# Performance work log

Hardware: AMD Instinct MI355X
Metric: run time of the kernel (lower is better)

Reference implementation:

```python
import jax, jax.numpy as jnp
import numpy as np
from jax import lax

CAM_EDGE = 4096


def setup_inputs() -> dict:
    key = jax.random.key(0)
    x1 = jax.random.normal(key, (CAM_EDGE, CAM_EDGE), dtype=jnp.float32)
    return {"x1": x1}


def _label_components(mask):
    """4-connected component labeling via iterative min-label propagation.

    mask: [E, E] bool. Returns int32 [E, E] labels: each masked cell gets the
    minimum linear index of its connected component; unmasked cells get the
    sentinel N = E*E.
    """
    E = mask.shape[0]
    N = E * E
    sent = jnp.int32(N)
    init = jnp.where(mask, jnp.arange(N, dtype=jnp.int32).reshape(E, E), sent)
    sent_row = jnp.full((1, E), sent, dtype=jnp.int32)
    sent_col = jnp.full((E, 1), sent, dtype=jnp.int32)

    def propagate(lab):
        dn = jnp.concatenate([sent_row, lab[:-1]], axis=0)   # neighbor from above
        up = jnp.concatenate([lab[1:], sent_row], axis=0)    # neighbor from below
        lf = jnp.concatenate([sent_col, lab[:, :-1]], axis=1)
        rt = jnp.concatenate([lab[:, 1:], sent_col], axis=1)
        m = jnp.minimum(jnp.minimum(lab, up), jnp.minimum(dn, jnp.minimum(lf, rt)))
        return jnp.where(mask, m, sent)

    def cond(carry):
        _, changed = carry
        return changed

    def body(carry):
        lab, _ = carry
        new = propagate(lab)
        return new, jnp.any(new != lab)

    labels, _ = lax.while_loop(cond, body, (init, jnp.array(True)))
    return labels


def reference(x1):
    E = x1.shape[0]
    N = E * E
    v = jnp.tanh(x1)
    mask = v > 0
    labels = _label_components(mask)          # [E, E] int32, sentinel N for masked-out
    flat_lab = labels.reshape(-1)
    vflat = jnp.where(mask, v, 0.0).reshape(-1)
    ones = mask.reshape(-1).astype(v.dtype)
    # bucket N+1 collects the sentinel (non-positive cells); drop it
    sums = jax.ops.segment_sum(vflat, flat_lab, num_segments=N + 1)[:N]
    counts = jax.ops.segment_sum(ones, flat_lab, num_segments=N + 1)[:N]
    has = counts > 0                          # one True per connected component (its root index)
    per_comp = jnp.where(has, sums / (N + 1 - counts), 0.0)
    n_comp = jnp.sum(has.astype(v.dtype))
    total = jnp.sum(per_comp)
    return jnp.where(n_comp > 0, total / n_comp, 0.0)
```

## Files before the change

kernel.cpp:

```cpp
#include <hip/hip_runtime.h>

#define EDGE 4096
#define NPIX (EDGE * EDGE)
#define NTILES 4096
#define SLOTS 2048
#define PREP_BLOCKS 2048

typedef unsigned long long u64;

static __device__ __forceinline__ int g_load(int* L, int i) {
    return __hip_atomic_load(&L[i], __ATOMIC_RELAXED, __HIP_MEMORY_SCOPE_AGENT);
}
static __device__ __forceinline__ void g_store(int* L, int i, int v) {
    __hip_atomic_store(&L[i], v, __ATOMIC_RELAXED, __HIP_MEMORY_SCOPE_AGENT);
}
static __device__ int g_find(int* L, int i) {
    while (true) {
        const int p = g_load(L, i);
        if (p == i) return i;
        const int gp = g_load(L, p);
        if (gp == p) return p;
        g_store(L, i, gp);
        i = gp;
    }
}
static __device__ int g_unite(int* L, int a, int b) {
    while (true) {
        a = g_find(L, a); b = g_find(L, b);
        if (a == b) return 0;
        const int lo = a < b ? a : b;
        const int hi = a ^ b ^ lo;
        const int old = atomicMin(&L[hi], lo);
        if (old == hi) return 1;
        a = lo; b = old;
    }
}

static __device__ __forceinline__ int l_load(int* L, int i) {
    return __hip_atomic_load(&L[i], __ATOMIC_RELAXED, __HIP_MEMORY_SCOPE_WORKGROUP);
}
static __device__ __forceinline__ void l_store(int* L, int i, int v) {
    __hip_atomic_store(&L[i], v, __ATOMIC_RELAXED, __HIP_MEMORY_SCOPE_WORKGROUP);
}
static __device__ int l_find(int* L, int i) {
    while (true) {
        const int p = l_load(L, i);
        if (p == i) return i;
        const int gp = l_load(L, p);
        if (gp == p) return p;
        l_store(L, i, gp);
        i = gp;
    }
}
static __device__ void l_unite(int* L, int a, int b) {
    while (true) {
        a = l_find(L, a); b = l_find(L, b);
        if (a == b) return;
        const int lo = a < b ? a : b;
        const int hi = a ^ b ^ lo;
        const int old = atomicMin(&L[hi], lo);
        if (old == hi) return;
        a = lo; b = old;
    }
}

__global__ __launch_bounds__(256) void k_prep(const float* __restrict__ x,
                                              unsigned char* __restrict__ maskb,
                                              double* __restrict__ partials) {
    __shared__ float wsumf[4];
    float sf = 0.0f;
    const int stride = gridDim.x * blockDim.x;
    for (int p = blockIdx.x * blockDim.x + threadIdx.x; p < NPIX / 8; p += stride) {
        const float4 a0 = reinterpret_cast<const float4*>(x)[p * 2];
        const float4 a1 = reinterpret_cast<const float4*>(x)[p * 2 + 1];
        const float v[8] = {a0.x, a0.y, a0.z, a0.w, a1.x, a1.y, a1.z, a1.w};
        unsigned int m = 0;
        #pragma unroll
        for (int j = 0; j < 8; ++j) {
            const float vj = v[j];
            if (vj > 0.0f) {
                m |= 1u << j;
                const float e = __expf(2.0f * vj);
                sf += 1.0f - 2.0f * __builtin_amdgcn_rcpf(e + 1.0f);
            }
        }
        maskb[p] = (unsigned char)m;
    }
    for (int off = 32; off > 0; off >>= 1) sf += __shfl_down(sf, off, 64);
    if ((threadIdx.x & 63) == 0) wsumf[threadIdx.x >> 6] = sf;
    __syncthreads();
    if (threadIdx.x == 0)
        partials[blockIdx.x] =
            (double)wsumf[0] + (double)wsumf[1] + (double)wsumf[2] + (double)wsumf[3];
}

__global__ __launch_bounds__(256) void k_ccl(const u64* __restrict__ M,
                                             int* __restrict__ G,
                                             int* __restrict__ topM, int* __restrict__ botM,
                                             int* __restrict__ leftM, int* __restrict__ rightM,
                                             int* __restrict__ rootsArr) {
    __shared__ u64 mrow[64];
    __shared__ u64 rstart[64];
    __shared__ int rowbase[64];
    __shared__ int P[SLOTS];
    __shared__ int wtot[4];
    __shared__ int Rtot;
    const int t = threadIdx.x;
    const int tile = blockIdx.x;
    const int tr = tile >> 6, tc = tile & 63;

    if (t < 64) {
        const u64 m = M[(((tr << 6) | t) << 6) | tc];
        mrow[t] = m;
        const u64 rs = m & ~(m << 1);
        rstart[t] = rs;
        int inc = __popcll(rs);
        const int nr = inc;
        #pragma unroll
        for (int off = 1; off < 64; off <<= 1) {
            const int v = __shfl_up(inc, off, 64);
            if (t >= off) inc += v;
        }
        rowbase[t] = inc - nr;
        if (t == 63) Rtot = inc;
    }
    #pragma unroll
    for (int i = t; i < SLOTS; i += 256) P[i] = i;
    __syncthreads();

    {
        const int rr = t >> 2;
        if (rr >= 1) {
            const u64 vm = mrow[rr] & mrow[rr - 1];
            u64 st = vm & ~(vm << 1);
            const int cb = (t & 3) * 16;
            st = (st >> cb) & 0xFFFFull;
            if (st) {
                const u64 rs  = rstart[rr];
                const u64 rsu = rstart[rr - 1];
                const int rb  = rowbase[rr];
                const int rbu = rowbase[rr - 1];
                do {
                    const int j = __builtin_ctzll(st) + cb;
                    const u64 thru = ~0ull >> (63 - j);
                    const int na = rb  + __popcll(rs  & thru) - 1;
                    const int nb = rbu + __popcll(rsu & thru) - 1;
                    const int old = atomicMin(&P[na], nb);
                    if (old != na && old != nb) l_unite(P, nb, old);
                    st &= st - 1;
                } while (st);
            }
        }
    }
    __syncthreads();

    const int R = Rtot;
    int broot = -1;
    {
        int rr, j;
        if (t < 64)       { rr = 0;       j = t; }
        else if (t < 128) { rr = 63;      j = t - 64; }
        else if (t < 192) { rr = t - 128; j = 0; }
        else              { rr = t - 192; j = 63; }
        if ((mrow[rr] >> j) & 1ull) {
            const int idx = __popcll(rstart[rr] & (~0ull >> (63 - j))) - 1;
            broot = l_find(P, rowbase[rr] + idx);
        }
    }
    int c = 0;
    for (int i = t; i < R; i += 256) c += (P[i] == i);
    int inc2 = c;
    #pragma unroll
    for (int off = 1; off < 64; off <<= 1) {
        const int v = __shfl_up(inc2, off, 64);
        if ((t & 63) >= off) inc2 += v;
    }
    if ((t & 63) == 63) wtot[t >> 6] = inc2;
    __syncthreads();

    const int w = t >> 6;
    int wbase = 0;
    if (w > 0) wbase += wtot[0];
    if (w > 1) wbase += wtot[1];
    if (w > 2) wbase += wtot[2];
    const int my_base = wbase + inc2 - c;
    const int nroots = wtot[0] + wtot[1] + wtot[2] + wtot[3];
    const int tileBase = tile * SLOTS;
    {
        int k = my_base;
        for (int i = t; i < R; i += 256) if (P[i] == i) P[i] = k++;
    }
    for (int i = t; i < nroots; i += 256) G[tileBase + i] = tileBase + i;
    __syncthreads();

    {
        const int node = (broot >= 0) ? (tileBase + P[broot]) : -1;
        const int bi = (tile << 6) | (t & 63);
        if (t < 64)       topM[bi]   = node;
        else if (t < 128) botM[bi]   = node;
        else if (t < 192) leftM[bi]  = node;
        else              rightM[bi] = node;
    }
    if (t == 0) rootsArr[tile] = nroots;
}

__global__ __launch_bounds__(128) void k_xmerge(const int* __restrict__ topM,
                                                const int* __restrict__ botM,
                                                const int* __restrict__ leftM,
                                                const int* __restrict__ rightM,
                                                int* G, int* __restrict__ linksArr) {
    __shared__ int lsum[2];
    const int t = threadIdx.x, tile = blockIdx.x;
    const int tr = tile >> 6, tc = tile & 63;
    int links = 0;
    if (t < 64) {
        if (tr > 0) {
            const int a = topM[(tile << 6) | t];
            const int b = botM[((tile - 64) << 6) | t];
            const int ap = __shfl_up(a, 1, 64);
            const int bp = __shfl_up(b, 1, 64);
            if ((a | b) >= 0) {
                const bool redund = (t > 0) && ((ap | bp) >= 0);
                if (!redund) links = g_unite(G, a, b);
            }
        }
    } else {
        const int rr = t - 64;
        if (tc > 0) {
            const int a = leftM[(tile << 6) | rr];
            const int b = rightM[((tile - 1) << 6) | rr];
            const int ap = __shfl_up(a, 1, 64);
            const int bp = __shfl_up(b, 1, 64);
            if ((a | b) >= 0) {
                const bool redund = (rr > 0) && ((ap | bp) >= 0);
                if (!redund) links = g_unite(G, a, b);
            }
        }
    }
    for (int off = 32; off > 0; off >>= 1) links += __shfl_down(links, off, 64);
    if ((t & 63) == 0) lsum[t >> 6] = links;
    __syncthreads();
    if (t == 0) linksArr[tile] = lsum[0] + lsum[1];
}

__global__ __launch_bounds__(256) void k_final(const double* __restrict__ partials,
                                               const int* __restrict__ rootsArr,
                                               const int* __restrict__ linksArr,
                                               float* __restrict__ out) {
    __shared__ double sd[256];
    __shared__ int si[256];
    const int t = threadIdx.x;
    double s = 0.0; int n = 0;
    for (int i = t; i < PREP_BLOCKS; i += 256) s += partials[i];
    for (int i = t; i < NTILES; i += 256) n += rootsArr[i] - linksArr[i];
    sd[t] = s; si[t] = n; __syncthreads();
    for (int off = 128; off > 0; off >>= 1) {
        if (t < off) { sd[t] += sd[t + off]; si[t] += si[t + off]; }
        __syncthreads();
    }
    if (t == 0) {
        const int nn = si[0];
        out[0] = (nn > 0) ? (float)(sd[0] / (double)(NPIX + 1) / (double)nn) : 0.0f;
    }
}

extern "C" void kernel_launch(void* const* d_in, const int* in_sizes, int n_in,
                              void* d_out, int out_size, void* d_ws, size_t ws_size,
                              hipStream_t stream) {
    const float* x = (const float*)d_in[0];
    float* out = (float*)d_out;

    char* ws = (char*)d_ws;
    int* G = (int*)ws;
    int* topM   = (int*)(ws + (32u << 20));
    int* botM   = topM  + NTILES * 64;
    int* leftM  = botM  + NTILES * 64;
    int* rightM = leftM + NTILES * 64;
    unsigned char* maskb = (unsigned char*)(ws + (36u << 20));
    double* partials = (double*)(ws + (38u << 20));
    int* rootsArr = (int*)(ws + (38u << 20) + (64u << 10));
    int* linksArr = (int*)(ws + (38u << 20) + (80u << 10));

    k_prep  <<<PREP_BLOCKS, 256, 0, stream>>>(x, maskb, partials);
    k_ccl   <<<NTILES, 256, 0, stream>>>((const u64*)maskb, G,
                                         topM, botM, leftM, rightM, rootsArr);
    k_xmerge<<<NTILES, 128, 0, stream>>>(topM, botM, leftM, rightM, G, linksArr);
    k_final <<<1, 256, 0, stream>>>(partials, rootsArr, linksArr, out);
}
```

Baseline: 59.51 us.

## Process one tile per wavefront in CCL and merge, with tile-major mask layout

The prep kernel now writes the bit mask in a tile-major layout, so each tile's 64 row words sit next to each other and load in one coalesced read. The local labeling kernel now gives each 64x64 tile to a single wavefront, four tiles per block. Row data moves between lanes by shuffle instead of shared memory, and wave barriers replace block-wide __syncthreads. The cross-tile merge kernel also handles one tile per wave, with each lane doing both the vertical and horizontal edges. This removes block synchronisation and raises work per block, but each wave now serialises the row-union loop that four threads per row used to share, and it uses 32KB of LDS per block.

```diff
diff --git a/kernel.cpp b/kernel.cpp
--- a/kernel.cpp
+++ b/kernel.cpp
@@ -84,7 +84,9 @@
                 sf += 1.0f - 2.0f * __builtin_amdgcn_rcpf(e + 1.0f);
             }
         }
-        maskb[p] = (unsigned char)m;
+        const int row = p >> 9, cp = p & 511;
+        const int tile = ((row >> 6) << 6) | (cp >> 3);
+        maskb[((size_t)tile << 9) | ((row & 63) << 3) | (cp & 7)] = (unsigned char)m;
     }
     for (int off = 32; off > 0; off >>= 1) sf += __shfl_down(sf, off, 64);
     if ((threadIdx.x & 63) == 0) wsumf[threadIdx.x >> 6] = sf;
@@ -99,148 +101,111 @@
                                              int* __restrict__ topM, int* __restrict__ botM,
                                              int* __restrict__ leftM, int* __restrict__ rightM,
                                              int* __restrict__ rootsArr) {
-    __shared__ u64 mrow[64];
-    __shared__ u64 rstart[64];
-    __shared__ int rowbase[64];
-    __shared__ int P[SLOTS];
-    __shared__ int wtot[4];
-    __shared__ int Rtot;
-    const int t = threadIdx.x;
-    const int tile = blockIdx.x;
-    const int tr = tile >> 6, tc = tile & 63;
-
-    if (t < 64) {
-        const u64 m = M[(((tr << 6) | t) << 6) | tc];
-        mrow[t] = m;
-        const u64 rs = m & ~(m << 1);
-        rstart[t] = rs;
-        int inc = __popcll(rs);
-        const int nr = inc;
-        #pragma unroll
-        for (int off = 1; off < 64; off <<= 1) {
-            const int v = __shfl_up(inc, off, 64);
-            if (t >= off) inc += v;
-        }
-        rowbase[t] = inc - nr;
-        if (t == 63) Rtot = inc;
-    }
+    __shared__ int Pall[4][SLOTS];
+    const int lane = threadIdx.x & 63;
+    const int w = threadIdx.x >> 6;
+    const int tile = (blockIdx.x << 2) | w;
+    int* P = Pall[w];
+
+    const u64 m = M[(tile << 6) | lane];
+    const u64 rs = m & ~(m << 1);
+    const int nr = __popcll(rs);
+    int inc = nr;
     #pragma unroll
-    for (int i = t; i < SLOTS; i += 256) P[i] = i;
-    __syncthreads();
-
-    {
-        const int rr = t >> 2;
-        if (rr >= 1) {
-            const u64 vm = mrow[rr] & mrow[rr - 1];
-            u64 st = vm & ~(vm << 1);
-            const int cb = (t & 3) * 16;
-            st = (st >> cb) & 0xFFFFull;
-            if (st) {
-                const u64 rs  = rstart[rr];
-                const u64 rsu = rstart[rr - 1];
-                const int rb  = rowbase[rr];
-                const int rbu = rowbase[rr - 1];
-                do {
-                    const int j = __builtin_ctzll(st) + cb;
-                    const u64 thru = ~0ull >> (63 - j);
-                    const int na = rb  + __popcll(rs  & thru) - 1;
-                    const int nb = rbu + __popcll(rsu & thru) - 1;
-                    const int old = atomicMin(&P[na], nb);
-                    if (old != na && old != nb) l_unite(P, nb, old);
-                    st &= st - 1;
-                } while (st);
-            }
-        }
-    }
-    __syncthreads();
-
-    const int R = Rtot;
-    int broot = -1;
-    {
-        int rr, j;
-        if (t < 64)       { rr = 0;       j = t; }
-        else if (t < 128) { rr = 63;      j = t - 64; }
-        else if (t < 192) { rr = t - 128; j = 0; }
-        else              { rr = t - 192; j = 63; }
-        if ((mrow[rr] >> j) & 1ull) {
-            const int idx = __popcll(rstart[rr] & (~0ull >> (63 - j))) - 1;
-            broot = l_find(P, rowbase[rr] + idx);
-        }
-    }
+    for (int off = 1; off < 64; off <<= 1) {
+        const int v = __shfl_up(inc, off, 64);
+        if (lane >= off) inc += v;
+    }
+    const int rowbase = inc - nr;
+    const int R = __shfl(inc, 63, 64);
+
+    #pragma unroll
+    for (int q = 0; q < SLOTS / 64; ++q) P[(q << 6) | lane] = (q << 6) | lane;
+    __builtin_amdgcn_wave_barrier();
+
+    const u64 mu  = __shfl_up(m, 1, 64);
+    const u64 rsu = __shfl_up(rs, 1, 64);
+    const int rbu = __shfl_up(rowbase, 1, 64);
+    if (lane >= 1) {
+        const u64 vm = m & mu;
+        u64 st = vm & ~(vm << 1);
+        while (st) {
+            const int j = __builtin_ctzll(st);
+            const u64 thru = ~0ull >> (63 - j);
+            const int na = rowbase + __popcll(rs  & thru) - 1;
+            const int nb = rbu     + __popcll(rsu & thru) - 1;
+            const int old = atomicMin(&P[na], nb);
+            if (old != na && old != nb) l_unite(P, nb, old);
+            st &= st - 1;
+        }
+    }
+    __builtin_amdgcn_wave_barrier();
+
+    const u64 m0  = __shfl((long long)m, 0, 64),  rs0  = __shfl((long long)rs, 0, 64);
+    const u64 m63 = __shfl((long long)m, 63, 64), rs63 = __shfl((long long)rs, 63, 64);
+    const int rb63 = __shfl(rowbase, 63, 64);
+    const u64 thruL = ~0ull >> (63 - lane);
+    int bt = -1, bb = -1, bl = -1, br = -1;
+    if ((m0 >> lane) & 1ull)  bt = l_find(P, __popcll(rs0 & thruL) - 1);
+    if ((m63 >> lane) & 1ull) bb = l_find(P, rb63 + __popcll(rs63 & thruL) - 1);
+    if (m & 1ull)             bl = l_find(P, rowbase);
+    if ((m >> 63) & 1ull)     br = l_find(P, rowbase + nr - 1);
+    __builtin_amdgcn_wave_barrier();
+
     int c = 0;
-    for (int i = t; i < R; i += 256) c += (P[i] == i);
+    for (int i = lane; i < R; i += 64) c += (P[i] == i);
     int inc2 = c;
     #pragma unroll
     for (int off = 1; off < 64; off <<= 1) {
         const int v = __shfl_up(inc2, off, 64);
-        if ((t & 63) >= off) inc2 += v;
-    }
-    if ((t & 63) == 63) wtot[t >> 6] = inc2;
-    __syncthreads();
-
-    const int w = t >> 6;
-    int wbase = 0;
-    if (w > 0) wbase += wtot[0];
-    if (w > 1) wbase += wtot[1];
-    if (w > 2) wbase += wtot[2];
-    const int my_base = wbase + inc2 - c;
-    const int nroots = wtot[0] + wtot[1] + wtot[2] + wtot[3];
+        if (lane >= off) inc2 += v;
+    }
+    const int nroots = __shfl(inc2, 63, 64);
+    int k = inc2 - c;
+    for (int i = lane; i < R; i += 64) if (P[i] == i) P[i] = k++;
+    __builtin_amdgcn_wave_barrier();
+
     const int tileBase = tile * SLOTS;
-    {
-        int k = my_base;
-        for (int i = t; i < R; i += 256) if (P[i] == i) P[i] = k++;
-    }
-    for (int i = t; i < nroots; i += 256) G[tileBase + i] = tileBase + i;
-    __syncthreads();
-
-    {
-        const int node = (broot >= 0) ? (tileBase + P[broot]) : -1;
-        const int bi = (tile << 6) | (t & 63);
-        if (t < 64)       topM[bi]   = node;
-        else if (t < 128) botM[bi]   = node;
-        else if (t < 192) leftM[bi]  = node;
-        else              rightM[bi] = node;
-    }
-    if (t == 0) rootsArr[tile] = nroots;
-}
-
-__global__ __launch_bounds__(128) void k_xmerge(const int* __restrict__ topM,
+    for (int i = lane; i < nroots; i += 64) G[tileBase + i] = tileBase + i;
+
+    const int bi = (tile << 6) | lane;
+    topM[bi]   = (bt >= 0) ? (tileBase + P[bt]) : -1;
+    botM[bi]   = (bb >= 0) ? (tileBase + P[bb]) : -1;
+    leftM[bi]  = (bl >= 0) ? (tileBase + P[bl]) : -1;
+    rightM[bi] = (br >= 0) ? (tileBase + P[br]) : -1;
+    if (lane == 0) rootsArr[tile] = nroots;
+}
+
+__global__ __launch_bounds__(256) void k_xmerge(const int* __restrict__ topM,
                                                 const int* __restrict__ botM,
                                                 const int* __restrict__ leftM,
                                                 const int* __restrict__ rightM,
                                                 int* G, int* __restrict__ linksArr) {
-    __shared__ int lsum[2];
-    const int t = threadIdx.x, tile = blockIdx.x;
+    const int lane = threadIdx.x & 63;
+    const int w = threadIdx.x >> 6;
+    const int tile = (blockIdx.x << 2) | w;
     const int tr = tile >> 6, tc = tile & 63;
     int links = 0;
-    if (t < 64) {
-        if (tr > 0) {
-            const int a = topM[(tile << 6) | t];
-            const int b = botM[((tile - 64) << 6) | t];
-            const int ap = __shfl_up(a, 1, 64);
-            const int bp = __shfl_up(b, 1, 64);
-            if ((a | b) >= 0) {
-                const bool redund = (t > 0) && ((ap | bp) >= 0);
-                if (!redund) links = g_unite(G, a, b);
-            }
-        }
-    } else {
-        const int rr = t - 64;
-        if (tc > 0) {
-            const int a = leftM[(tile << 6) | rr];
-            const int b = rightM[((tile - 1) << 6) | rr];
-            const int ap = __shfl_up(a, 1, 64);
-            const int bp = __shfl_up(b, 1, 64);
-            if ((a | b) >= 0) {
-                const bool redund = (rr > 0) && ((ap | bp) >= 0);
-                if (!redund) links = g_unite(G, a, b);
-            }
+    {
+        int a = -1, b = -1;
+        if (tr > 0) { a = topM[(tile << 6) | lane]; b = botM[((tile - 64) << 6) | lane]; }
+        const int ap = __shfl_up(a, 1, 64), bp = __shfl_up(b, 1, 64);
+        if (tr > 0 && (a | b) >= 0) {
+            const bool red = (lane > 0) && ((ap | bp) >= 0);
+            if (!red) links += g_unite(G, a, b);
+        }
+    }
+    {
+        int a = -1, b = -1;
+        if (tc > 0) { a = leftM[(tile << 6) | lane]; b = rightM[((tile - 1) << 6) | lane]; }
+        const int ap = __shfl_up(a, 1, 64), bp = __shfl_up(b, 1, 64);
+        if (tc > 0 && (a | b) >= 0) {
+            const bool red = (lane > 0) && ((ap | bp) >= 0);
+            if (!red) links += g_unite(G, a, b);
         }
     }
     for (int off = 32; off > 0; off >>= 1) links += __shfl_down(links, off, 64);
-    if ((t & 63) == 0) lsum[t >> 6] = links;
-    __syncthreads();
-    if (t == 0) linksArr[tile] = lsum[0] + lsum[1];
+    if (lane == 0) linksArr[tile] = links;
 }
 
 __global__ __launch_bounds__(256) void k_final(const double* __restrict__ partials,
@@ -282,8 +247,8 @@
     int* linksArr = (int*)(ws + (38u << 20) + (80u << 10));
 
     k_prep  <<<PREP_BLOCKS, 256, 0, stream>>>(x, maskb, partials);
-    k_ccl   <<<NTILES, 256, 0, stream>>>((const u64*)maskb, G,
-                                         topM, botM, leftM, rightM, rootsArr);
-    k_xmerge<<<NTILES, 128, 0, stream>>>(topM, botM, leftM, rightM, G, linksArr);
+    k_ccl   <<<NTILES / 4, 256, 0, stream>>>((const u64*)maskb, G,
+                                             topM, botM, leftM, rightM, rootsArr);
+    k_xmerge<<<NTILES / 4, 256, 0, stream>>>(topM, botM, leftM, rightM, G, linksArr);
     k_final <<<1, 256, 0, stream>>>(partials, rootsArr, linksArr, out);
 }
```

New measurement: 64.64 us. 8.6% more time.
